# Performance work log

Measured on AMD Instinct MI355X. Metric: run time of the kernel, lower is better.

The kernel has to match this reference:

```python
import math
import jax, jax.numpy as jnp
import numpy as np

D = 768      # hidden_size
H = 16       # num_attention_heads (hardcoded in module)
DH = D // H  # value dim per head
SEQ = 512    # fpos/tpos are taken modulo 512
EPS = 1e-5   # torch LayerNorm default
SCALE = math.sqrt(D / H)  # attention_head_size = dim_key_query_all / num_heads


def _collab_attn(h, fpos, tpos, Wq, Wk, Wcb, Wv, bv, mix, Wd, bd, lng, lnb):
    """CollaborativeAttention.forward on one segment. h: [SEQ, D]."""
    fpos = fpos % SEQ
    tpos = tpos % SEQ
    fs = h[fpos]                                   # [F, D] gathered 'from' nodes
    ts = h[tpos]                                   # [T, D] gathered 'to' nodes
    q = fs @ Wq.T                                  # [F, D] (no bias)
    k = ts @ Wk.T                                  # [T, D] (no bias)
    mq = q[None, :, :] * mix[:, None, :]           # [H, F, D] per-head mixing
    scores = jnp.einsum('hfd,td->hft', mq, k)      # [H, F, T] full-D contraction
    cb = (ts @ Wcb.T).T                            # [H, T] content bias
    scores = (scores + cb[:, None, :]) / SCALE
    probs = jax.nn.softmax(scores, axis=-1)        # dropout = identity at eval
    v = (ts @ Wv.T + bv).reshape(-1, H, DH).transpose(1, 0, 2)  # [H, T, DH]
    ctx = jnp.einsum('hft,htd->hfd', probs, v)     # [H, F, DH]
    ctx = ctx.transpose(1, 0, 2).reshape(-1, D) @ Wd.T + bd      # [F, D]
    x = fs + ctx                                   # residual on gathered nodes
    mu = x.mean(-1, keepdims=True)
    var = ((x - mu) ** 2).mean(-1, keepdims=True)
    return lng * (x - mu) / jnp.sqrt(var + EPS) + lnb


def _encoder(hidden_states, fpos, tpos, qtoc, ctoq):
    outs = []
    for b in range(3):  # fixed small segment count, matches original unrolling
        o1 = _collab_attn(hidden_states[b], fpos[b], tpos[b], *qtoc).mean(0)
        o2 = _collab_attn(hidden_states[b], tpos[b], fpos[b], *ctoq).mean(0)
        outs.append(jnp.concatenate([o1, o2]))
    return jnp.stack(outs)  # [3, 2*D]


def setup_inputs() -> dict:
    key = jax.random.key(0)
    ks = jax.random.split(key, 32)
    inp = {
        'hidden_states': jax.random.normal(ks[0], (3, SEQ, D), jnp.float32),
        'fpos': jax.random.randint(ks[1], (3, 2048), 0, SEQ, jnp.int32),
        'tpos': jax.random.randint(ks[2], (3, 2048), 0, SEQ, jnp.int32),
    }
    i = 3
    for p in ('qtoc', 'ctoq'):
        for n, shape, std in (('Wq', (D, D), 0.02), ('Wk', (D, D), 0.02),
                              ('Wcb', (H, D), 0.02), ('Wv', (D, D), 0.02),
                              ('Wd', (D, D), 0.02), ('mix', (H, D), 0.2)):
            inp[p + '_' + n] = std * jax.random.normal(ks[i], shape, jnp.float32)
            i += 1
        inp[p + '_bv'] = jnp.zeros((D,), jnp.float32)
        inp[p + '_bd'] = jnp.zeros((D,), jnp.float32)
        inp[p + '_lng'] = jnp.ones((D,), jnp.float32)
        inp[p + '_lnb'] = jnp.zeros((D,), jnp.float32)
    return inp


def reference(hidden_states, fpos, tpos,
              qtoc_Wq, qtoc_Wk, qtoc_Wcb, qtoc_Wv, qtoc_Wd, qtoc_mix,
              qtoc_bv, qtoc_bd, qtoc_lng, qtoc_lnb,
              ctoq_Wq, ctoq_Wk, ctoq_Wcb, ctoq_Wv, ctoq_Wd, ctoq_mix,
              ctoq_bv, ctoq_bd, ctoq_lng, ctoq_lnb):
    qtoc = (qtoc_Wq, qtoc_Wk, qtoc_Wcb, qtoc_Wv, qtoc_bv, qtoc_mix,
            qtoc_Wd, qtoc_bd, qtoc_lng, qtoc_lnb)
    ctoq = (ctoq_Wq, ctoq_Wk, ctoq_Wcb, ctoq_Wv, ctoq_bv, ctoq_mix,
            ctoq_Wd, ctoq_bd, ctoq_lng, ctoq_lnb)
    return _encoder(hidden_states, fpos, tpos, qtoc, ctoq)
```

## Files before the change

### kernel.cpp

```cpp
#include <hip/hip_runtime.h>
#include <math.h>

#define DD 768
#define HH 16
#define DHH 48
#define NPOS 512
#define NIDX 2048
#define INV_SCALE 0.14433756729740643f
#define LN_EPS 1e-5f

typedef __bf16 bf16_t;
typedef __bf16 bf16x8 __attribute__((ext_vector_type(8)));
typedef float f32x4 __attribute__((ext_vector_type(4)));

__device__ __forceinline__ void g2lds16(const void* g, void* l) {
  __builtin_amdgcn_global_load_lds((const __attribute__((address_space(1))) void*)g,
                                   (__attribute__((address_space(3))) void*)l, 16, 0, 0);
}
__device__ __forceinline__ int stg_chunk(int lane) { return (lane & 3) ^ ((lane >> 3) & 3); }
__device__ __forceinline__ int rd_off(int row, int lq) {
  return row * 32 + ((lq ^ ((row >> 1) & 3)) << 3);
}

struct CvtDesc { const float* src; bf16_t* dst; int n8; };
struct CvtBatch { CvtDesc d[13]; };

__global__ __launch_bounds__(256) void prep(const int* __restrict__ fpos,
                                            const int* __restrict__ tpos,
                                            int* __restrict__ CNT, CvtBatch cvb) {
  const int bid = blockIdx.x;
  const int tid = threadIdx.x;
  __shared__ int shist[NPOS];
  if (bid < 6) {
    const int b = bid >> 1, which = bid & 1;
    const int* src = (which ? tpos : fpos) + b * NIDX;
    for (int i = tid; i < NPOS; i += 256) shist[i] = 0;
    __syncthreads();
    for (int i = tid; i < NIDX; i += 256) atomicAdd(&shist[src[i] & (NPOS - 1)], 1);
    __syncthreads();
    for (int i = tid; i < NPOS; i += 256) CNT[bid * NPOS + i] = shist[i];
    return;
  }
  const CvtDesc de = cvb.d[(bid - 6) >> 6];
  for (int i = ((bid - 6) & 63) * 256 + tid; i < de.n8; i += 64 * 256) {
    bf16_t t[8];
    if (de.src) {
      const f32x4 a = *(const f32x4*)(de.src + (size_t)i * 8);
      const f32x4 b = *(const f32x4*)(de.src + (size_t)i * 8 + 4);
#pragma unroll
      for (int e = 0; e < 4; ++e) { t[e] = (bf16_t)a[e]; t[4 + e] = (bf16_t)b[e]; }
    } else {
#pragma unroll
      for (int e = 0; e < 8; ++e) t[e] = (bf16_t)0.f;
    }
    *(bf16x8*)(de.dst + (size_t)i * 8) = *(bf16x8*)t;
  }
}

__global__ __launch_bounds__(256) void qmix(const bf16_t* __restrict__ Qbf,
                                            const float* __restrict__ mix0,
                                            const float* __restrict__ mix1,
                                            bf16_t* __restrict__ Qm) {
  const int idx = blockIdx.x * 256 + threadIdx.x;
  const int c = idx % 96;
  const int f = (idx / 96) & 511;
  const int h = (idx / (96 * 512)) & 15;
  const int pd = idx / (96 * 512 * 16);
  const bf16x8 q = *(const bf16x8*)(Qbf + ((size_t)pd * NPOS + f) * DD + c * 8);
  const float* m = ((pd & 1) ? mix1 : mix0) + h * DD + c * 8;
  const f32x4 m0 = *(const f32x4*)m;
  const f32x4 m1 = *(const f32x4*)(m + 4);
  bf16_t t[8];
#pragma unroll
  for (int e = 0; e < 4; ++e) {
    t[e]     = (bf16_t)((float)q[e] * m0[e] * INV_SCALE);
    t[4 + e] = (bf16_t)((float)q[4 + e] * m1[e] * INV_SCALE);
  }
  *(bf16x8*)(Qm + ((size_t)(pd * 16 + h) * NPOS + f) * DD + c * 8) = *(bf16x8*)t;
}

struct MDesc { const bf16_t* A; const bf16_t* B; const float* bias; void* C;
               float* cb; int mode; int ntiles; };
struct MBatch { MDesc d[18]; };

__global__ __launch_bounds__(256, 4) void gemm64(MBatch batch) {
  const MDesc de = batch.d[blockIdx.y];
  const int mt = blockIdx.x & 7, nt = blockIdx.x >> 3;
  if (nt >= de.ntiles) return;
  const int m0 = mt * 64, n0 = nt * 128;

  __shared__ bf16_t SA[2][2048];
  __shared__ bf16_t SB[2][4096];

  const int tid = threadIdx.x;
  const int w = tid >> 6, lane = tid & 63;
  const int wm = w >> 1, wn = w & 1;
  const int lm = lane & 15, lq = lane >> 4;
  const int sr = lane >> 2, sc = stg_chunk(lane);

  f32x4 acc[2][4] = {};

  auto stage = [&](int buf, int k0) {
#pragma unroll
    for (int c = 0; c < 3; ++c) {
      const int issue = w + c * 4;
      if (issue < 4)
        g2lds16(de.A + (size_t)(m0 + issue * 16 + sr) * 768 + k0 + sc * 8,
                SA[buf] + issue * 512);
      else {
        const int e = issue - 4;
        g2lds16(de.B + (size_t)(n0 + e * 16 + sr) * 768 + k0 + sc * 8,
                SB[buf] + e * 512);
      }
    }
  };

  stage(0, 0);
  for (int k0i = 0; k0i < 24; ++k0i) {
    const int cur = k0i & 1;
    __syncthreads();
    if (k0i + 1 < 24) stage(cur ^ 1, (k0i + 1) * 32);
    bf16x8 af[2], bfr[4];
#pragma unroll
    for (int i = 0; i < 2; ++i)
      af[i] = *(const bf16x8*)(SA[cur] + rd_off(wm * 32 + i * 16 + lm, lq));
#pragma unroll
    for (int j = 0; j < 4; ++j)
      bfr[j] = *(const bf16x8*)(SB[cur] + rd_off(wn * 64 + j * 16 + lm, lq));
#pragma unroll
    for (int i = 0; i < 2; ++i)
#pragma unroll
      for (int j = 0; j < 4; ++j)
        acc[i][j] = __builtin_amdgcn_mfma_f32_16x16x32_bf16(af[i], bfr[j], acc[i][j], 0, 0, 0);
  }

#pragma unroll
  for (int i = 0; i < 2; ++i) {
    const int rbase = m0 + wm * 32 + i * 16 + lq * 4;
#pragma unroll
    for (int j = 0; j < 4; ++j) {
      const int c = n0 + wn * 64 + j * 16 + lm;
      const float bv = (de.bias && c < 768) ? de.bias[c] : 0.f;
#pragma unroll
      for (int r = 0; r < 4; ++r) {
        const float v = acc[i][j][r] + bv;
        if (de.mode == 0)      ((float*)de.C)[(size_t)(rbase + r) * 768 + c] = v;
        else if (de.mode == 1) ((bf16_t*)de.C)[(size_t)(rbase + r) * 768 + c] = (bf16_t)v;
        else if (de.mode == 2) ((bf16_t*)de.C)[(size_t)c * NPOS + rbase + r] = (bf16_t)v;
        else {
          if (c < 768)       ((bf16_t*)de.C)[(size_t)(rbase + r) * 768 + c] = (bf16_t)v;
          else if (c < 784)  de.cb[(size_t)(rbase + r) * 16 + (c - 768)] = v;
        }
      }
    }
  }
}

template <int PRE>
__global__ __launch_bounds__(256, 3) void attn_mfma(
    const bf16_t* __restrict__ Qg, const bf16_t* __restrict__ Qm,
    const bf16_t* __restrict__ Kg, const bf16_t* __restrict__ Vt,
    const float* __restrict__ cbG, const int* __restrict__ CNT,
    const float* __restrict__ mix0, const float* __restrict__ mix1,
    bf16_t* __restrict__ CTX) {
  const int bid = blockIdx.x;
  const int ft = bid & 7, h = (bid >> 3) & 15, pd = bid >> 7;
  const int dir = pd & 1;
  const int f0 = ft * 64;

  __shared__ bf16_t U[17408];
  __shared__ float mixs[PRE ? 4 : 768];
  __shared__ float cbw[512];
  __shared__ float rowl[64];

  const int tid = threadIdx.x;
  const int w = tid >> 6, lane = tid & 63;
  const bf16_t* Qp = PRE ? (Qm + (size_t)(pd * 16 + h) * NPOS * DD)
                         : (Qg + (size_t)pd * NPOS * DD);
  const bf16_t* Kp = Kg + (size_t)pd * NPOS * DD;
  const bf16_t* Vp = Vt + (size_t)pd * DD * NPOS + (size_t)h * DHH * NPOS;
  const int* cnt = CNT + ((pd & ~1) + (1 - dir)) * NPOS;

  if (!PRE) {
    const float* mix = (dir ? mix1 : mix0) + h * DD;
    for (int i = tid; i < 768; i += 256) mixs[i] = mix[i] * INV_SCALE;
  }
  for (int i = tid; i < 512; i += 256)
    cbw[i] = cbG[((size_t)pd * NPOS + i) * HH + h] * INV_SCALE + __logf((float)cnt[i]);

  const int wm = w >> 1, wn = w & 1;
  const int lm = lane & 15, lq = lane >> 4;
  const int sr = lane >> 2, sc = stg_chunk(lane);

  f32x4 pv[4] = {};

  for (int jt = 0; jt < 4; ++jt) {
    const int j0 = jt * 128;
    __syncthreads();

    auto stage = [&](int buf, int k0) {
#pragma unroll
      for (int c = 0; c < 3; ++c) {
        const int issue = w + c * 4;
        if (issue < 4)
          g2lds16(Qp + (size_t)(f0 + issue * 16 + sr) * DD + k0 + sc * 8,
                  U + buf * 6144 + issue * 512);
        else {
          const int e = issue - 4;
          g2lds16(Kp + (size_t)(j0 + e * 16 + sr) * DD + k0 + sc * 8,
                  U + buf * 6144 + 2048 + e * 512);
        }
      }
    };

    stage(0, 0);
    f32x4 sa[2][4] = {};
    for (int k0i = 0; k0i < 24; ++k0i) {
      const int cur = k0i & 1;
      const int k0 = k0i * 32;
      __syncthreads();
      if (k0i + 1 < 24) stage(cur ^ 1, k0 + 32);
      bf16x8 af[2], bfr[4];
#pragma unroll
      for (int i = 0; i < 2; ++i) {
        const int off = cur * 6144 + rd_off(wm * 32 + i * 16 + lm, lq);
        if (PRE) {
          af[i] = *(const bf16x8*)(U + off);
        } else {
          const f32x4 mxa = *(const f32x4*)&mixs[k0 + lq * 8];
          const f32x4 mxb = *(const f32x4*)&mixs[k0 + lq * 8 + 4];
          const bf16x8 q = *(const bf16x8*)(U + off);
          bf16_t t[8];
#pragma unroll
          for (int e = 0; e < 4; ++e) {
            t[e]     = (bf16_t)((float)q[e] * mxa[e]);
            t[4 + e] = (bf16_t)((float)q[4 + e] * mxb[e]);
          }
          af[i] = *(bf16x8*)t;
        }
      }
#pragma unroll
      for (int j = 0; j < 4; ++j)
        bfr[j] = *(const bf16x8*)(U + cur * 6144 + 2048 + rd_off(wn * 64 + j * 16 + lm, lq));
#pragma unroll
      for (int i = 0; i < 2; ++i)
#pragma unroll
        for (int j = 0; j < 4; ++j)
          sa[i][j] = __builtin_amdgcn_mfma_f32_16x16x32_bf16(af[i], bfr[j], sa[i][j], 0, 0, 0);
    }
    __syncthreads();

#pragma unroll
    for (int j = 0; j < 4; ++j) {
      const int col = wn * 64 + j * 16 + lm;
      const float cb = cbw[j0 + col];
#pragma unroll
      for (int i = 0; i < 2; ++i) {
        const int rbase = wm * 32 + i * 16 + lq * 4;
#pragma unroll
        for (int r = 0; r < 4; ++r)
          U[(rbase + r) * 136 + col] = (bf16_t)__expf(sa[i][j][r] + cb);
      }
    }
    for (int i = tid; i < 49 * 16; i += 256) {
      const int r = i >> 4, cc = i & 15;
      if (r < 48)
        *(bf16x8*)(U + 8704 + r * 136 + cc * 8) =
            *(const bf16x8*)(Vp + (size_t)r * NPOS + j0 + cc * 8);
      else {
        bf16_t ones[8];
#pragma unroll
        for (int e = 0; e < 8; ++e) ones[e] = (bf16_t)1.f;
        *(bf16x8*)(U + 8704 + 48 * 136 + cc * 8) = *(bf16x8*)ones;
      }
    }
    __syncthreads();

#pragma unroll
    for (int kk = 0; kk < 4; ++kk) {
      const bf16x8 pa = *(const bf16x8*)(U + (w * 16 + lm) * 136 + kk * 32 + lq * 8);
#pragma unroll
      for (int j = 0; j < 4; ++j) {
        const bf16x8 pb = *(const bf16x8*)(U + 8704 + (j * 16 + lm) * 136 + kk * 32 + lq * 8);
        pv[j] = __builtin_amdgcn_mfma_f32_16x16x32_bf16(pa, pb, pv[j], 0, 0, 0);
      }
    }
  }

  if (lm == 0) {
#pragma unroll
    for (int r = 0; r < 4; ++r) rowl[w * 16 + lq * 4 + r] = pv[3][r];
  }
  __syncthreads();
#pragma unroll
  for (int j = 0; j < 3; ++j) {
#pragma unroll
    for (int r = 0; r < 4; ++r) {
      const int fr = w * 16 + lq * 4 + r;
      CTX[((size_t)pd * NPOS + f0 + fr) * DD + h * DHH + j * 16 + lm] =
          (bf16_t)(pv[j][r] / rowl[fr]);
    }
  }
}

__global__ __launch_bounds__(256) void ln_mean_kernel(
    const float* __restrict__ hs, const float* __restrict__ XB,
    const int* __restrict__ CNT,
    const float* __restrict__ lng0, const float* __restrict__ lnb0,
    const float* __restrict__ lng1, const float* __restrict__ lnb1,
    float* __restrict__ out) {
  const int blk = blockIdx.x;
  const int chunk = blk & 63;
  const int pd = blk >> 6;
  const int b = pd >> 1, dir = pd & 1;
  const float* lng = dir ? lng1 : lng0;
  const float* lnb = dir ? lnb1 : lnb0;
  const int* cnt = CNT + pd * NPOS;
  const float* hb = hs + (size_t)b * NPOS * DD;
  const float* xb = XB + (size_t)pd * NPOS * DD;

  __shared__ float wacc[4][DD];
  const int tid = threadIdx.x;
  const int wave = tid >> 6, lane = tid & 63;
  for (int d0 = tid; d0 < 4 * DD; d0 += 256) ((float*)wacc)[d0] = 0.f;
  __syncthreads();

  float lg[12], lb[12];
#pragma unroll
  for (int qd = 0; qd < 12; ++qd) {
    lg[qd] = lng[lane + qd * 64];
    lb[qd] = lnb[lane + qd * 64];
  }

  for (int rr = 0; rr < 2; ++rr) {
    const int p = chunk * 8 + wave * 2 + rr;
    float x[12];
    float s = 0.f, ss = 0.f;
#pragma unroll
    for (int qd = 0; qd < 12; ++qd) {
      const int d0 = lane + qd * 64;
      const float xv = hb[(size_t)p * DD + d0] + xb[(size_t)p * DD + d0];
      x[qd] = xv; s += xv; ss += xv * xv;
    }
#pragma unroll
    for (int o = 1; o < 64; o <<= 1) {
      s += __shfl_xor(s, o);
      ss += __shfl_xor(ss, o);
    }
    const float mu = s * (1.f / 768.f);
    const float var = ss * (1.f / 768.f) - mu * mu;
    const float rstd = rsqrtf(var + LN_EPS);
    const float wgt = (float)cnt[p];
    if (wgt != 0.f) {
#pragma unroll
      for (int qd = 0; qd < 12; ++qd) {
        const int d0 = lane + qd * 64;
        wacc[wave][d0] += wgt * (lg[qd] * (x[qd] - mu) * rstd + lb[qd]);
      }
    }
  }
  __syncthreads();
  for (int d0 = tid; d0 < DD; d0 += 256) {
    const float t = wacc[0][d0] + wacc[1][d0] + wacc[2][d0] + wacc[3][d0];
    atomicAdd(&out[b * 1536 + dir * 768 + d0], t * (1.f / 2048.f));
  }
}

extern "C" void kernel_launch(void* const* d_in, const int* in_sizes, int n_in,
                              void* d_out, int out_size, void* d_ws, size_t ws_size,
                              hipStream_t stream) {
  const float* hs  = (const float*)d_in[0];
  const int* fpos  = (const int*)d_in[1];
  const int* tpos  = (const int*)d_in[2];

  const float* Wq[2]; const float* Wk[2]; const float* Wcb[2]; const float* Wv[2];
  const float* Wd[2]; const float* mixp[2];
  const float* bv[2]; const float* bd[2]; const float* lng[2]; const float* lnb[2];
  for (int p = 0; p < 2; ++p) {
    const int base = 3 + p * 10;
    Wq[p]   = (const float*)d_in[base + 0];
    Wk[p]   = (const float*)d_in[base + 1];
    Wcb[p]  = (const float*)d_in[base + 2];
    Wv[p]   = (const float*)d_in[base + 3];
    Wd[p]   = (const float*)d_in[base + 4];
    mixp[p] = (const float*)d_in[base + 5];
    bv[p]   = (const float*)d_in[base + 6];
    bd[p]   = (const float*)d_in[base + 7];
    lng[p]  = (const float*)d_in[base + 8];
    lnb[p]  = (const float*)d_in[base + 9];
  }

  char* wsp = (char*)d_ws;
  size_t off = 0;
  auto alloc = [&](size_t bytes) { char* p = wsp + off; off = (off + bytes + 255) & ~(size_t)255; return p; };
  bf16_t* hsb  = (bf16_t*)alloc((size_t)3 * NPOS * DD * 2);
  bf16_t* Wb   = (bf16_t*)alloc((size_t)6 * DD * DD * 2);
  bf16_t* WkCb = (bf16_t*)alloc((size_t)2 * 896 * DD * 2);
  bf16_t* Qbf  = (bf16_t*)alloc((size_t)6 * NPOS * DD * 2);
  bf16_t* Kbf  = (bf16_t*)alloc((size_t)6 * NPOS * DD * 2);
  bf16_t* VtG  = (bf16_t*)alloc((size_t)6 * DD * NPOS * 2);
  bf16_t* CTXb = (bf16_t*)alloc((size_t)6 * NPOS * DD * 2);
  float*  XB   = (float*) alloc((size_t)6 * NPOS * DD * 4);
  float*  cbG  = (float*) alloc((size_t)6 * NPOS * HH * 4);
  int*    CNTb = (int*)   alloc((size_t)6 * NPOS * 4);
  const size_t qm_bytes = (size_t)6 * HH * NPOS * DD * 2;
  const int use_pre = (off + qm_bytes + 4096 <= ws_size);
  bf16_t* Qm = use_pre ? (bf16_t*)alloc(qm_bytes) : nullptr;

  hipMemsetAsync(d_out, 0, (size_t)out_size * sizeof(float), stream);

  CvtBatch cvb{};
  cvb.d[0] = CvtDesc{hs, hsb, 3 * NPOS * DD / 8};
  for (int p = 0; p < 2; ++p) {
    cvb.d[1 + p * 3] = CvtDesc{Wq[p], Wb + (size_t)(p * 3 + 0) * DD * DD, DD * DD / 8};
    cvb.d[2 + p * 3] = CvtDesc{Wv[p], Wb + (size_t)(p * 3 + 1) * DD * DD, DD * DD / 8};
    cvb.d[3 + p * 3] = CvtDesc{Wd[p], Wb + (size_t)(p * 3 + 2) * DD * DD, DD * DD / 8};
    bf16_t* wk = WkCb + (size_t)p * 896 * DD;
    cvb.d[7 + p * 3] = CvtDesc{Wk[p], wk, DD * DD / 8};
    cvb.d[8 + p * 3] = CvtDesc{Wcb[p], wk + (size_t)768 * DD, 16 * DD / 8};
    cvb.d[9 + p * 3] = CvtDesc{nullptr, wk + (size_t)784 * DD, 112 * DD / 8};
  }
  prep<<<838, 256, 0, stream>>>(fpos, tpos, CNTb, cvb);

  MBatch gb{};
  int n = 0;
  for (int b = 0; b < 3; ++b)
    for (int p = 0; p < 2; ++p) {
      const int pd = b * 2 + p;
      const bf16_t* A = hsb + (size_t)b * NPOS * DD;
      const size_t o = (size_t)pd * NPOS * DD;
      gb.d[n++] = MDesc{A, Wb + (size_t)(p * 3 + 0) * DD * DD, nullptr, Qbf + o, nullptr, 1, 6};
      gb.d[n++] = MDesc{A, WkCb + (size_t)p * 896 * DD, nullptr, Kbf + o,
                        cbG + (size_t)pd * NPOS * HH, 3, 7};
      gb.d[n++] = MDesc{A, Wb + (size_t)(p * 3 + 1) * DD * DD, bv[p],
                        VtG + (size_t)pd * DD * NPOS, nullptr, 2, 6};
    }
  gemm64<<<dim3(56, 18), 256, 0, stream>>>(gb);

  if (use_pre) {
    qmix<<<18432, 256, 0, stream>>>(Qbf, mixp[0], mixp[1], Qm);
    attn_mfma<1><<<768, 256, 0, stream>>>(Qbf, Qm, Kbf, VtG, cbG, CNTb,
                                          mixp[0], mixp[1], CTXb);
  } else {
    attn_mfma<0><<<768, 256, 0, stream>>>(Qbf, Qbf, Kbf, VtG, cbG, CNTb,
                                          mixp[0], mixp[1], CTXb);
  }

  MBatch gd{};
  for (int b = 0; b < 3; ++b)
    for (int p = 0; p < 2; ++p) {
      const int pd = b * 2 + p;
      const size_t o = (size_t)pd * NPOS * DD;
      gd.d[pd] = MDesc{CTXb + o, Wb + (size_t)(p * 3 + 2) * DD * DD, bd[p],
                       XB + o, nullptr, 0, 6};
    }
  gemm64<<<dim3(56, 6), 256, 0, stream>>>(gd);

  ln_mean_kernel<<<384, 256, 0, stream>>>(hs, XB, CNTb, lng[0], lnb[0], lng[1], lnb[1],
                                          (float*)d_out);
}
```

Before: 260.3 us.

## Compute full score tile in one pass per wave and drop precomputed mixed-Q

Removes the qmix kernel and the large per-head mixed-Q buffer, and applies the mix on the fly in the attention kernel instead. The QK loop is restructured so that each wave computes scores for 64 rows against its own 128 key columns in a single K sweep. This stages Q once rather than once per key tile, with accumulators held in 32 registers. Waves then take turns writing exp(scores) for their key tile into shared memory for the PV step. The cost is higher register pressure, larger LDS (occupancy bound dropped to 2), and serialized exp writes, one wave per key tile.

```diff
diff --git a/kernel.cpp b/kernel.cpp
--- a/kernel.cpp
+++ b/kernel.cpp
@@ -57,28 +57,6 @@
   }
 }
 
-__global__ __launch_bounds__(256) void qmix(const bf16_t* __restrict__ Qbf,
-                                            const float* __restrict__ mix0,
-                                            const float* __restrict__ mix1,
-                                            bf16_t* __restrict__ Qm) {
-  const int idx = blockIdx.x * 256 + threadIdx.x;
-  const int c = idx % 96;
-  const int f = (idx / 96) & 511;
-  const int h = (idx / (96 * 512)) & 15;
-  const int pd = idx / (96 * 512 * 16);
-  const bf16x8 q = *(const bf16x8*)(Qbf + ((size_t)pd * NPOS + f) * DD + c * 8);
-  const float* m = ((pd & 1) ? mix1 : mix0) + h * DD + c * 8;
-  const f32x4 m0 = *(const f32x4*)m;
-  const f32x4 m1 = *(const f32x4*)(m + 4);
-  bf16_t t[8];
-#pragma unroll
-  for (int e = 0; e < 4; ++e) {
-    t[e]     = (bf16_t)((float)q[e] * m0[e] * INV_SCALE);
-    t[4 + e] = (bf16_t)((float)q[4 + e] * m1[e] * INV_SCALE);
-  }
-  *(bf16x8*)(Qm + ((size_t)(pd * 16 + h) * NPOS + f) * DD + c * 8) = *(bf16x8*)t;
-}
-
 struct MDesc { const bf16_t* A; const bf16_t* B; const float* bias; void* C;
                float* cb; int mode; int ntiles; };
 struct MBatch { MDesc d[18]; };
@@ -156,112 +134,90 @@
   }
 }
 
-template <int PRE>
-__global__ __launch_bounds__(256, 3) void attn_mfma(
-    const bf16_t* __restrict__ Qg, const bf16_t* __restrict__ Qm,
-    const bf16_t* __restrict__ Kg, const bf16_t* __restrict__ Vt,
-    const float* __restrict__ cbG, const int* __restrict__ CNT,
-    const float* __restrict__ mix0, const float* __restrict__ mix1,
-    bf16_t* __restrict__ CTX) {
+__global__ __launch_bounds__(256, 2) void attn_mfma(
+    const bf16_t* __restrict__ Qg, const bf16_t* __restrict__ Kg,
+    const bf16_t* __restrict__ Vt, const float* __restrict__ cbG,
+    const int* __restrict__ CNT, const float* __restrict__ mix0,
+    const float* __restrict__ mix1, bf16_t* __restrict__ CTX) {
   const int bid = blockIdx.x;
   const int ft = bid & 7, h = (bid >> 3) & 15, pd = bid >> 7;
   const int dir = pd & 1;
   const int f0 = ft * 64;
 
-  __shared__ bf16_t U[17408];
-  __shared__ float mixs[PRE ? 4 : 768];
+  __shared__ bf16_t U[36864];
+  __shared__ float mixs[768];
   __shared__ float cbw[512];
   __shared__ float rowl[64];
 
   const int tid = threadIdx.x;
   const int w = tid >> 6, lane = tid & 63;
-  const bf16_t* Qp = PRE ? (Qm + (size_t)(pd * 16 + h) * NPOS * DD)
-                         : (Qg + (size_t)pd * NPOS * DD);
+  const bf16_t* Qp = Qg + (size_t)pd * NPOS * DD;
   const bf16_t* Kp = Kg + (size_t)pd * NPOS * DD;
   const bf16_t* Vp = Vt + (size_t)pd * DD * NPOS + (size_t)h * DHH * NPOS;
+  const float* mix = (dir ? mix1 : mix0) + h * DD;
   const int* cnt = CNT + ((pd & ~1) + (1 - dir)) * NPOS;
 
-  if (!PRE) {
-    const float* mix = (dir ? mix1 : mix0) + h * DD;
-    for (int i = tid; i < 768; i += 256) mixs[i] = mix[i] * INV_SCALE;
-  }
+  for (int i = tid; i < 768; i += 256) mixs[i] = mix[i] * INV_SCALE;
   for (int i = tid; i < 512; i += 256)
     cbw[i] = cbG[((size_t)pd * NPOS + i) * HH + h] * INV_SCALE + __logf((float)cnt[i]);
 
-  const int wm = w >> 1, wn = w & 1;
   const int lm = lane & 15, lq = lane >> 4;
   const int sr = lane >> 2, sc = stg_chunk(lane);
 
+  int qoff[4], koff[8];
+#pragma unroll
+  for (int i = 0; i < 4; ++i) qoff[i] = rd_off(i * 16 + lm, lq);
+#pragma unroll
+  for (int j = 0; j < 8; ++j) koff[j] = 2048 + w * 4096 + rd_off(j * 16 + lm, lq);
+
+  auto stage = [&](int buf, int k0) {
+    bf16_t* base = U + buf * 18432;
+    g2lds16(Qp + (size_t)(f0 + w * 16 + sr) * DD + k0 + sc * 8, base + w * 512);
+#pragma unroll
+    for (int e = 0; e < 8; ++e)
+      g2lds16(Kp + (size_t)(w * 128 + e * 16 + sr) * DD + k0 + sc * 8,
+              base + 2048 + w * 4096 + e * 512);
+  };
+
+  f32x4 sa[32];
+#pragma unroll
+  for (int t = 0; t < 32; ++t) sa[t] = (f32x4){0.f, 0.f, 0.f, 0.f};
+
+  stage(0, 0);
+  for (int k0i = 0; k0i < 24; ++k0i) {
+    const int cur = k0i & 1;
+    __syncthreads();
+    if (k0i + 1 < 24) stage(cur ^ 1, (k0i + 1) * 32);
+    const bf16_t* base = U + cur * 18432;
+    const int k0 = k0i * 32;
+    const f32x4 mxa = *(const f32x4*)&mixs[k0 + lq * 8];
+    const f32x4 mxb = *(const f32x4*)&mixs[k0 + lq * 8 + 4];
+    bf16x8 af[4];
+#pragma unroll
+    for (int i = 0; i < 4; ++i) {
+      const bf16x8 q = *(const bf16x8*)(base + qoff[i]);
+      bf16_t t[8];
+#pragma unroll
+      for (int e = 0; e < 4; ++e) {
+        t[e]     = (bf16_t)((float)q[e] * mxa[e]);
+        t[4 + e] = (bf16_t)((float)q[4 + e] * mxb[e]);
+      }
+      af[i] = *(bf16x8*)t;
+    }
+#pragma unroll
+    for (int j = 0; j < 8; ++j) {
+      const bf16x8 bf = *(const bf16x8*)(base + koff[j]);
+#pragma unroll
+      for (int i = 0; i < 4; ++i)
+        sa[i * 8 + j] = __builtin_amdgcn_mfma_f32_16x16x32_bf16(af[i], bf, sa[i * 8 + j], 0, 0, 0);
+    }
+  }
+
   f32x4 pv[4] = {};
-
   for (int jt = 0; jt < 4; ++jt) {
     const int j0 = jt * 128;
     __syncthreads();
 
-    auto stage = [&](int buf, int k0) {
-#pragma unroll
-      for (int c = 0; c < 3; ++c) {
-        const int issue = w + c * 4;
-        if (issue < 4)
-          g2lds16(Qp + (size_t)(f0 + issue * 16 + sr) * DD + k0 + sc * 8,
-                  U + buf * 6144 + issue * 512);
-        else {
-          const int e = issue - 4;
-          g2lds16(Kp + (size_t)(j0 + e * 16 + sr) * DD + k0 + sc * 8,
-                  U + buf * 6144 + 2048 + e * 512);
-        }
-      }
-    };
-
-    stage(0, 0);
-    f32x4 sa[2][4] = {};
-    for (int k0i = 0; k0i < 24; ++k0i) {
-      const int cur = k0i & 1;
-      const int k0 = k0i * 32;
-      __syncthreads();
-      if (k0i + 1 < 24) stage(cur ^ 1, k0 + 32);
-      bf16x8 af[2], bfr[4];
-#pragma unroll
-      for (int i = 0; i < 2; ++i) {
-        const int off = cur * 6144 + rd_off(wm * 32 + i * 16 + lm, lq);
-        if (PRE) {
-          af[i] = *(const bf16x8*)(U + off);
-        } else {
-          const f32x4 mxa = *(const f32x4*)&mixs[k0 + lq * 8];
-          const f32x4 mxb = *(const f32x4*)&mixs[k0 + lq * 8 + 4];
-          const bf16x8 q = *(const bf16x8*)(U + off);
-          bf16_t t[8];
-#pragma unroll
-          for (int e = 0; e < 4; ++e) {
-            t[e]     = (bf16_t)((float)q[e] * mxa[e]);
-            t[4 + e] = (bf16_t)((float)q[4 + e] * mxb[e]);
-          }
-          af[i] = *(bf16x8*)t;
-        }
-      }
-#pragma unroll
-      for (int j = 0; j < 4; ++j)
-        bfr[j] = *(const bf16x8*)(U + cur * 6144 + 2048 + rd_off(wn * 64 + j * 16 + lm, lq));
-#pragma unroll
-      for (int i = 0; i < 2; ++i)
-#pragma unroll
-        for (int j = 0; j < 4; ++j)
-          sa[i][j] = __builtin_amdgcn_mfma_f32_16x16x32_bf16(af[i], bfr[j], sa[i][j], 0, 0, 0);
-    }
-    __syncthreads();
-
-#pragma unroll
-    for (int j = 0; j < 4; ++j) {
-      const int col = wn * 64 + j * 16 + lm;
-      const float cb = cbw[j0 + col];
-#pragma unroll
-      for (int i = 0; i < 2; ++i) {
-        const int rbase = wm * 32 + i * 16 + lq * 4;
-#pragma unroll
-        for (int r = 0; r < 4; ++r)
-          U[(rbase + r) * 136 + col] = (bf16_t)__expf(sa[i][j][r] + cb);
-      }
-    }
     for (int i = tid; i < 49 * 16; i += 256) {
       const int r = i >> 4, cc = i & 15;
       if (r < 48)
@@ -272,6 +228,20 @@
 #pragma unroll
         for (int e = 0; e < 8; ++e) ones[e] = (bf16_t)1.f;
         *(bf16x8*)(U + 8704 + 48 * 136 + cc * 8) = *(bf16x8*)ones;
+      }
+    }
+    if (w == jt) {
+#pragma unroll
+      for (int jj = 0; jj < 8; ++jj) {
+        const int col = jj * 16 + lm;
+        const float cb = cbw[j0 + col];
+#pragma unroll
+        for (int i = 0; i < 4; ++i) {
+          const int rb = i * 16 + lq * 4;
+#pragma unroll
+          for (int r = 0; r < 4; ++r)
+            U[(rb + r) * 136 + col] = (bf16_t)__expf(sa[i * 8 + jj][r] + cb);
+        }
       }
     }
     __syncthreads();
@@ -403,9 +373,6 @@
   float*  XB   = (float*) alloc((size_t)6 * NPOS * DD * 4);
   float*  cbG  = (float*) alloc((size_t)6 * NPOS * HH * 4);
   int*    CNTb = (int*)   alloc((size_t)6 * NPOS * 4);
-  const size_t qm_bytes = (size_t)6 * HH * NPOS * DD * 2;
-  const int use_pre = (off + qm_bytes + 4096 <= ws_size);
-  bf16_t* Qm = use_pre ? (bf16_t*)alloc(qm_bytes) : nullptr;
 
   hipMemsetAsync(d_out, 0, (size_t)out_size * sizeof(float), stream);
 
@@ -437,14 +404,7 @@
     }
   gemm64<<<dim3(56, 18), 256, 0, stream>>>(gb);
 
-  if (use_pre) {
-    qmix<<<18432, 256, 0, stream>>>(Qbf, mixp[0], mixp[1], Qm);
-    attn_mfma<1><<<768, 256, 0, stream>>>(Qbf, Qm, Kbf, VtG, cbG, CNTb,
-                                          mixp[0], mixp[1], CTXb);
-  } else {
-    attn_mfma<0><<<768, 256, 0, stream>>>(Qbf, Qbf, Kbf, VtG, cbG, CNTb,
-                                          mixp[0], mixp[1], CTXb);
-  }
+  attn_mfma<<<768, 256, 0, stream>>>(Qbf, Kbf, VtG, cbG, CNTb, mixp[0], mixp[1], CTXb);
 
   MBatch gd{};
   for (int b = 0; b < 3; ++b)
```

Result: no change. 263.6 us (+1.3%).
